# Performance work log

Hardware: AMD Instinct MI355X
Metric: run time of the kernel (lower is better)

Reference implementation:

```python
import jax, jax.numpy as jnp
import numpy as np

SPH, SPW = 24, 24          # spatial tile size
NBLK = 2                   # channel blocks (in_channels // 512)
EPS = 1e-5


def _tiles(h, w):
    nh = int(np.ceil(h / SPH)); nw = int(np.ceil(w / SPW))
    sh = (h - SPH) // (nh - 1) if nh > 1 else 0
    sw = (w - SPW) // (nw - 1) if nw > 1 else 0
    offs = []
    for i in range(nh):
        for j in range(nw):
            offs.append((max(0, i * sh), max(0, j * sw)))
    return offs, nh, nw


def _mlp(x_v, w1, b1, w2, b2):
    # 1x1 conv1d pair over the spatial_area axis: x_v (B, S, C)
    h = jax.nn.relu(jnp.einsum('os,bsc->boc', w1, x_v) + b1[None, :, None])
    return jnp.einsum('so,boc->bsc', w2, h) + b2[None, :, None]


def _forward(x, w_in1, b_in1, w_in2, b_in2, w_out1, b_out1, w_out2, b_out2, bn_gamma, bn_beta):
    bt, c, h, w = x.shape
    offs, nh, nw = _tiles(h, w)
    # gather overlapping (here exactly tiling) spatial patches -> stacked chunk batch
    chunks = [x[:, :, ty:ty + SPH, tx:tx + SPW].reshape(bt, c, SPH * SPW) for ty, tx in offs]
    x_stacked = jnp.concatenate(chunks, 0)            # (nchunks*bt, c, S)
    x_v = jnp.transpose(x_stacked, (0, 2, 1))         # (B, S, c)
    x_v = _mlp(x_v, w_in1, b_in1, w_in2, b_in2)
    # negative squared-distance score over channel means (no detach in this branch)
    x_m = x_v.mean(axis=1)                            # (B, c)
    score = -(x_m[:, None, :] - x_m[:, :, None]) ** 2  # (B, c, c)
    blk = c // NBLK
    ids = jnp.arange(c) // blk
    mask = ids[:, None] == ids[None, :]               # block-diagonal channel mask
    score = jnp.where(mask[None], score, -jnp.inf)
    attn = jax.nn.softmax(score, axis=1)              # softmax over dim 1 (rows)
    out = jnp.einsum('bsc,bcd->bsd', x_v, attn)       # torch.bmm(x_v, attn)
    out = _mlp(out, w_out1, b_out1, w_out2, b_out2)
    # BatchNorm1d(spatial_area) in training mode: stats over (B, c) per S-channel
    mu = out.mean(axis=(0, 2), keepdims=True)
    var = out.var(axis=(0, 2), keepdims=True)
    out = (out - mu) * jax.lax.rsqrt(var + EPS) * bn_gamma[None, :, None] + bn_beta[None, :, None]
    out = jnp.transpose(out, (0, 2, 1))               # (B, c, S)
    # scatter_add chunks back (scaled by 1/spblock_h^2, as in the original)
    scale = 1.0 / (nh * nh)
    res = x
    for idx, (ty, tx) in enumerate(offs):
        chunk = out[idx * bt:(idx + 1) * bt].reshape(bt, c, SPH, SPW)
        res = res.at[:, :, ty:ty + SPH, tx:tx + SPW].add(chunk * scale)
    return jax.nn.relu(res)


def setup_inputs() -> dict:
    key = jax.random.key(0)
    ks = jax.random.split(key, 9)
    S = SPH * SPW          # 576
    H = S // 8             # 72 (reduction=8)
    s = 0.02
    return {
        'x': jax.random.normal(ks[0], (16, 1024, 48, 48), dtype=jnp.float32),
        'w_in1': jax.random.normal(ks[1], (H, S), dtype=jnp.float32) * s,
        'b_in1': jnp.zeros((H,), jnp.float32),
        'w_in2': jax.random.normal(ks[2], (S, H), dtype=jnp.float32) * s,
        'b_in2': jnp.zeros((S,), jnp.float32),
        'w_out1': jax.random.normal(ks[3], (H, S), dtype=jnp.float32) * s,
        'b_out1': jnp.zeros((H,), jnp.float32),
        'w_out2': jax.random.normal(ks[4], (S, H), dtype=jnp.float32) * s,
        'b_out2': jnp.zeros((S,), jnp.float32),
        'bn_gamma': jnp.ones((S,), jnp.float32),
        'bn_beta': jnp.zeros((S,), jnp.float32),
    }


def reference(x, w_in1, b_in1, w_in2, b_in2, w_out1, b_out1, w_out2, b_out2, bn_gamma, bn_beta):
    return _forward(x, w_in1, b_in1, w_in2, b_in2, w_out1, b_out1, w_out2, b_out2, bn_gamma, bn_beta)
```

## Files before the change

kernel.cpp:

```cpp
#include <hip/hip_runtime.h>
#include <hip/hip_bf16.h>


#define EPS 1e-5f

typedef __attribute__((ext_vector_type(8))) short short8;
typedef __attribute__((ext_vector_type(4))) short short4v;
typedef __attribute__((ext_vector_type(4))) float f32x4;
typedef __attribute__((ext_vector_type(4))) float float4v;

#define GLD_LDS(g, l) __builtin_amdgcn_global_load_lds( \
    (const __attribute__((address_space(1))) void*)(g), \
    (__attribute__((address_space(3))) void*)(l), 16, 0, 0)

static __device__ __forceinline__ unsigned short f2bu(float f) {
    union { __hip_bfloat16 h; unsigned short u; } cv;
    cv.h = __float2bfloat16(f);
    return cv.u;
}

__global__ void prep_k(const float* __restrict__ w_in1, const float* __restrict__ b_in1,
                       const float* __restrict__ w_in2, const float* __restrict__ w_out2,
                       __hip_bfloat16* __restrict__ w1p, __hip_bfloat16* __restrict__ w2op,
                       float* __restrict__ b1p)
{
    int i = blockIdx.x * 256 + threadIdx.x;
    if (i < 128 * 576) {
        int r = i / 576, c = i - r * 576;
        w1p[i] = __float2bfloat16(r < 72 ? w_in1[r * 576 + c] : 0.f);
    }
    if (i < 640 * 96) {
        int r = i / 96, c = i - r * 96;
        bool ok = (r < 576) && (c < 72);
        w2op[i] = __float2bfloat16(ok ? w_out2[r * 72 + c] : 0.f);
    }
    if (i < 128)
        b1p[i] = i < 72 ? b_in1[i] : 0.f;
}

__global__ void prepM_k(const float* __restrict__ w_out1, const float* __restrict__ w_in2,
                        const float* __restrict__ b_in2, const float* __restrict__ b_out1,
                        __hip_bfloat16* __restrict__ Mp, float* __restrict__ b1G)
{
    int i = blockIdx.x * 256 + threadIdx.x;
    if (i >= 128 * 96) return;
    int h = i / 96, k = i - h * 96;
    float m = 0.f;
    if (h < 72 && k < 72) {
        for (int s = 0; s < 576; ++s)
            m += w_out1[h * 576 + s] * w_in2[s * 72 + k];
    } else if (h == 72 && k < 72) {
        for (int s = 0; s < 576; ++s)
            m += w_in2[s * 72 + k];
    }
    Mp[i] = __float2bfloat16(m);
    if (k == 0) {
        float c = 0.f;
        if (h < 72)
            for (int s = 0; s < 576; ++s)
                c += w_out1[h * 576 + s] * b_in2[s];
        b1G[h] = (h < 72) ? b_out1[h] + c : 0.f;
    }
}

__global__ void extract_k(const float4v* __restrict__ x4, __hip_bfloat16* __restrict__ xv)
{
    int i = blockIdx.x * 256 + threadIdx.x;
    int s4 = i % 144;
    int m = i / 144;
    int c = m & 1023;
    int b = m >> 10;
    int n = b & 15, ti = b >> 4;
    int ty = (ti >> 1) * 24, tx = (ti & 1) * 24;
    int s = s4 * 4;
    int sy = s / 24, sx = s - sy * 24;
    float4v v = x4[((((n << 10) + c) * 48 + ty + sy) * 48 + tx + sx) >> 2];
    short4v pk;
    pk.x = (short)f2bu(v.x); pk.y = (short)f2bu(v.y);
    pk.z = (short)f2bu(v.z); pk.w = (short)f2bu(v.w);
    *(short4v*)(xv + (long)i * 4) = pk;
}

__global__ __launch_bounds__(256) void fused_mlp1(
    const unsigned short* __restrict__ A,
    const unsigned short* __restrict__ W1,
    const float* __restrict__ b1,
    const unsigned short* __restrict__ Mp,
    unsigned short* __restrict__ G,
    float* __restrict__ xm_raw)
{
    __shared__ __align__(16) unsigned short smem[4096 + 4096 + 13312];
    unsigned short* As = smem;
    unsigned short* Bs = smem + 4096;
    unsigned short* Hs = smem + 8192;

    const int m0 = blockIdx.x * 128;
    const int t = threadIdx.x;
    const int lane = t & 63, wave = t >> 6;
    const int wr = wave >> 1, wc = wave & 1;
    const int lrow = lane & 15, kq = (lane >> 4) * 8;
    const int cr = (lane >> 4) * 4;
    const int r0 = t >> 2, c0 = (t & 3) * 8;

    f32x4 acc[4][4];
    #pragma unroll
    for (int i = 0; i < 4; ++i)
        #pragma unroll
        for (int j = 0; j < 4; ++j)
            acc[i][j] = (f32x4){0.f, 0.f, 0.f, 0.f};

    for (int k0 = 0; k0 < 576; k0 += 32) {
        GLD_LDS(A + (long)(m0 + r0) * 576 + k0 + c0,      &As[t * 8]);
        GLD_LDS(A + (long)(m0 + r0 + 64) * 576 + k0 + c0, &As[(t + 256) * 8]);
        GLD_LDS(W1 + (long)r0 * 576 + k0 + c0,            &Bs[t * 8]);
        GLD_LDS(W1 + (long)(r0 + 64) * 576 + k0 + c0,     &Bs[(t + 256) * 8]);
        __syncthreads();
        short8 af[4], bf[4];
        #pragma unroll
        for (int i = 0; i < 4; ++i)
            af[i] = *(const short8*)&As[(wr * 64 + i * 16 + lrow) * 32 + kq];
        #pragma unroll
        for (int j = 0; j < 4; ++j)
            bf[j] = *(const short8*)&Bs[(wc * 64 + j * 16 + lrow) * 32 + kq];
        #pragma unroll
        for (int i = 0; i < 4; ++i)
            #pragma unroll
            for (int j = 0; j < 4; ++j)
                acc[i][j] = __builtin_amdgcn_mfma_f32_16x16x32_bf16(af[i], bf[j], acc[i][j], 0, 0, 0);
        __syncthreads();
    }

    #pragma unroll
    for (int j = 0; j < 4; ++j) {
        int col = wc * 64 + j * 16 + lrow;
        if (col < 96) {
            float bv = b1[col];
            #pragma unroll
            for (int i = 0; i < 4; ++i) {
                int row = wr * 64 + i * 16 + cr;
                #pragma unroll
                for (int r = 0; r < 4; ++r)
                    Hs[(row + r) * 104 + col] = f2bu(fmaxf(acc[i][j][r] + bv, 0.f));
            }
        }
    }
    __syncthreads();

    f32x4 gacc[4][4];
    #pragma unroll
    for (int i = 0; i < 4; ++i)
        #pragma unroll
        for (int j = 0; j < 4; ++j)
            gacc[i][j] = (f32x4){0.f, 0.f, 0.f, 0.f};

    for (int k0 = 0; k0 < 96; k0 += 32) {
        GLD_LDS(Mp + (long)r0 * 96 + k0 + c0,        &As[t * 8]);
        GLD_LDS(Mp + (long)(r0 + 64) * 96 + k0 + c0, &As[(t + 256) * 8]);
        __syncthreads();
        short8 af[4], bf[4];
        #pragma unroll
        for (int i = 0; i < 4; ++i)
            af[i] = *(const short8*)&As[(wr * 64 + i * 16 + lrow) * 32 + kq];
        #pragma unroll
        for (int j = 0; j < 4; ++j)
            bf[j] = *(const short8*)&Hs[(wc * 64 + j * 16 + lrow) * 104 + k0 + kq];
        #pragma unroll
        for (int i = 0; i < 4; ++i)
            #pragma unroll
            for (int j = 0; j < 4; ++j)
                gacc[i][j] = __builtin_amdgcn_mfma_f32_16x16x32_bf16(af[i], bf[j], gacc[i][j], 0, 0, 0);
        __syncthreads();
    }

    const int z = m0 >> 9, m_local = m0 & 511;
    unsigned short* Gz = G + (long)z * 128 * 512;

    #pragma unroll
    for (int j = 0; j < 4; ++j) {
        int cn = wc * 64 + j * 16 + lrow;
        #pragma unroll
        for (int i = 0; i < 4; ++i) {
            int h = wr * 64 + i * 16 + cr;
            #pragma unroll
            for (int r = 0; r < 4; ++r)
                Gz[(long)(h + r) * 512 + m_local + cn] = f2bu(gacc[i][j][r]);
        }
    }

    if (wr == 1 && cr == 8) {
        #pragma unroll
        for (int j = 0; j < 4; ++j)
            xm_raw[(long)z * 512 + m_local + wc * 64 + j * 16 + lrow] = gacc[0][j][0];
    }
}

__global__ void denom_k(const float* __restrict__ xm_raw, const float* __restrict__ b_in2,
                        float* __restrict__ xmn, float* __restrict__ invd)
{
    __shared__ float sx[512];
    __shared__ float red[256];
    int z = blockIdx.x;
    int t = threadIdx.x;
    float p = 0.f;
    for (int i = t; i < 576; i += 256) p += b_in2[i];
    red[t] = p; __syncthreads();
    for (int o = 128; o; o >>= 1) { if (t < o) red[t] += red[t + o]; __syncthreads(); }
    float btot = red[0];
    for (int i = t; i < 512; i += 256) {
        float m = (xm_raw[(long)z * 512 + i] + btot) * (1.f / 576.f);
        sx[i] = m;
        xmn[(long)z * 512 + i] = m;
    }
    __syncthreads();
    #pragma unroll
    for (int dd = 0; dd < 2; ++dd) {
        int d = t + dd * 256;
        float xd = sx[d], s = 0.f;
        for (int c = 0; c < 512; ++c) { float df = sx[c] - xd; s += __expf(-df * df); }
        invd[(long)z * 512 + d] = 1.f / s;
    }
}

__global__ __launch_bounds__(256) void fused_attn_mlp2(
    const unsigned short* __restrict__ G,
    const float* __restrict__ xmn, const float* __restrict__ invd,
    const float* __restrict__ b1,
    const unsigned short* __restrict__ W2,
    const float* __restrict__ b2,
    __hip_bfloat16* __restrict__ C,
    float* __restrict__ statsR)
{
    __shared__ __align__(16) unsigned short smem[4096 + 4096 + 13312];
    unsigned short* As = smem;
    unsigned short* Bs = smem + 4096;
    unsigned short* Hs = smem + 8192;
    __shared__ float sxm[512];
    __shared__ float sinv[128];

    int bid = blockIdx.x;
    int lb = (bid & 7) * 64 + (bid >> 3);
    int z = lb >> 2;
    const int m0 = (lb & 3) * 128;
    const int t = threadIdx.x;
    const int lane = t & 63, wave = t >> 6;
    const int wr = wave >> 1, wc = wave & 1;
    const int lrow = lane & 15, kq = (lane >> 4) * 8;
    const int cr = (lane >> 4) * 4;
    const int r0 = t >> 2, c0 = (t & 3) * 8;
    const unsigned short* Gz = G + (long)z * 128 * 512;

    for (int i = t; i < 512; i += 256) sxm[i] = xmn[(long)z * 512 + i];
    if (t < 128) sinv[t] = invd[(long)z * 512 + m0 + t];
    __syncthreads();

    const int dA = t >> 1, cbA = (t & 1) * 16;
    const float xd = sxm[m0 + dA];
    const float ivd = sinv[dA];

    f32x4 acc[4][4];
    #pragma unroll
    for (int i = 0; i < 4; ++i)
        #pragma unroll
        for (int j = 0; j < 4; ++j)
            acc[i][j] = (f32x4){0.f, 0.f, 0.f, 0.f};

    for (int k0 = 0; k0 < 512; k0 += 32) {
        GLD_LDS(Gz + (long)r0 * 512 + k0 + c0,        &Bs[t * 8]);
        GLD_LDS(Gz + (long)(r0 + 64) * 512 + k0 + c0, &Bs[(t + 256) * 8]);
        short8 pk0, pk1;
        #pragma unroll
        for (int e = 0; e < 8; ++e) {
            float d0 = sxm[k0 + cbA + e] - xd;
            pk0[e] = (short)f2bu(__expf(-d0 * d0) * ivd);
            float d1 = sxm[k0 + cbA + 8 + e] - xd;
            pk1[e] = (short)f2bu(__expf(-d1 * d1) * ivd);
        }
        *(short8*)&As[dA * 32 + cbA]     = pk0;
        *(short8*)&As[dA * 32 + cbA + 8] = pk1;
        __syncthreads();
        short8 af[4], bf[4];
        #pragma unroll
        for (int i = 0; i < 4; ++i)
            af[i] = *(const short8*)&As[(wr * 64 + i * 16 + lrow) * 32 + kq];
        #pragma unroll
        for (int j = 0; j < 4; ++j)
            bf[j] = *(const short8*)&Bs[(wc * 64 + j * 16 + lrow) * 32 + kq];
        #pragma unroll
        for (int i = 0; i < 4; ++i)
            #pragma unroll
            for (int j = 0; j < 4; ++j)
                acc[i][j] = __builtin_amdgcn_mfma_f32_16x16x32_bf16(af[i], bf[j], acc[i][j], 0, 0, 0);
        __syncthreads();
    }

    #pragma unroll
    for (int j = 0; j < 4; ++j) {
        int col = wc * 64 + j * 16 + lrow;
        if (col < 96) {
            float bv = b1[col];
            #pragma unroll
            for (int i = 0; i < 4; ++i) {
                int row = wr * 64 + i * 16 + cr;
                #pragma unroll
                for (int r = 0; r < 4; ++r)
                    Hs[(row + r) * 104 + col] = f2bu(fmaxf(acc[i][j][r] + bv, 0.f));
            }
        }
    }
    __syncthreads();

    const long mg = (long)z * 512 + m0;
    float* st = statsR + (bid & 7) * 1152;
    for (int n0 = 0; n0 < 640; n0 += 128) {
        f32x4 a2[4][4];
        #pragma unroll
        for (int i = 0; i < 4; ++i)
            #pragma unroll
            for (int j = 0; j < 4; ++j)
                a2[i][j] = (f32x4){0.f, 0.f, 0.f, 0.f};

        for (int k0 = 0; k0 < 96; k0 += 32) {
            GLD_LDS(W2 + (long)(n0 + r0) * 96 + k0 + c0,      &Bs[t * 8]);
            GLD_LDS(W2 + (long)(n0 + r0 + 64) * 96 + k0 + c0, &Bs[(t + 256) * 8]);
            __syncthreads();
            short8 af[4], bf[4];
            #pragma unroll
            for (int i = 0; i < 4; ++i)
                af[i] = *(const short8*)&Hs[(wr * 64 + i * 16 + lrow) * 104 + k0 + kq];
            #pragma unroll
            for (int j = 0; j < 4; ++j)
                bf[j] = *(const short8*)&Bs[(wc * 64 + j * 16 + lrow) * 32 + kq];
            #pragma unroll
            for (int i = 0; i < 4; ++i)
                #pragma unroll
                for (int j = 0; j < 4; ++j)
                    a2[i][j] = __builtin_amdgcn_mfma_f32_16x16x32_bf16(af[i], bf[j], a2[i][j], 0, 0, 0);
            __syncthreads();
        }

        #pragma unroll
        for (int j = 0; j < 4; ++j) {
            int col = n0 + wc * 64 + j * 16 + lrow;
            bool live = col < 576;
            float bv = live ? b2[col] : 0.f;
            float s1 = 0.f, s2 = 0.f;
            #pragma unroll
            for (int i = 0; i < 4; ++i) {
                long rowb = (mg + wr * 64 + i * 16 + cr) * 576;
                #pragma unroll
                for (int r = 0; r < 4; ++r) {
                    float v = a2[i][j][r] + bv;
                    s1 += v; s2 += v * v;
                    if (live) C[rowb + (long)r * 576 + col] = __float2bfloat16(v);
                }
            }
            s1 += __shfl_xor(s1, 16, 64); s1 += __shfl_xor(s1, 32, 64);
            s2 += __shfl_xor(s2, 16, 64); s2 += __shfl_xor(s2, 32, 64);
            if ((lane >> 4) == 0 && live) {
                atomicAdd(&st[col], s1);
                atomicAdd(&st[576 + col], s2);
            }
        }
    }
}

__global__ void bnfin_k(const float* __restrict__ statsR,
                        const float* __restrict__ gamma, const float* __restrict__ beta,
                        float* __restrict__ ab)
{
    int s = threadIdx.x;
    float sum = 0.f, sq = 0.f;
    #pragma unroll
    for (int r = 0; r < 8; ++r) {
        sum += statsR[r * 1152 + s];
        sq  += statsR[r * 1152 + 576 + s];
    }
    float mu = sum * (1.f / 65536.f);
    float var = sq * (1.f / 65536.f) - mu * mu;
    float a = gamma[s] * rsqrtf(var + EPS);
    ab[s] = a;
    ab[576 + s] = beta[s] - mu * a;
}

__global__ void final_k(const float4v* __restrict__ x4, const __hip_bfloat16* __restrict__ out3,
                        const float* __restrict__ ab, float4v* __restrict__ out4)
{
    int i = blockIdx.x * 256 + threadIdx.x;
    int xx4 = i % 12; int t = i / 12;
    int y = t % 48; t /= 48;
    int c = t & 1023; int n = t >> 10;
    int xx = xx4 * 4;
    int ti = (y / 24) * 2 + (xx / 24);
    int b = ti * 16 + n;
    int s = (y % 24) * 24 + (xx % 24);
    const __hip_bfloat16* o3 = out3 + (((long)b << 10) + c) * 576 + s;
    float4v xv = x4[i];
    float4v o;
    #pragma unroll
    for (int e = 0; e < 4; ++e) {
        float v = __bfloat162float(o3[e]);
        float bn = v * ab[s + e] + ab[576 + s + e];
        float r = (e == 0 ? xv.x : e == 1 ? xv.y : e == 2 ? xv.z : xv.w) + 0.25f * bn;
        if (e == 0) o.x = fmaxf(r, 0.f);
        else if (e == 1) o.y = fmaxf(r, 0.f);
        else if (e == 2) o.z = fmaxf(r, 0.f);
        else o.w = fmaxf(r, 0.f);
    }
    out4[i] = o;
}

extern "C" void kernel_launch(void* const* d_in, const int* in_sizes, int n_in,
                              void* d_out, int out_size, void* d_ws, size_t ws_size,
                              hipStream_t stream)
{
    const float* x      = (const float*)d_in[0];
    const float* w_in1  = (const float*)d_in[1];
    const float* b_in1  = (const float*)d_in[2];
    const float* w_in2  = (const float*)d_in[3];
    const float* b_in2  = (const float*)d_in[4];
    const float* w_out1 = (const float*)d_in[5];
    const float* b_out1 = (const float*)d_in[6];
    const float* w_out2 = (const float*)d_in[7];
    const float* b_out2 = (const float*)d_in[8];
    const float* gamma  = (const float*)d_in[9];
    const float* beta   = (const float*)d_in[10];

    char* ws = (char*)d_ws;
    __hip_bfloat16* xv0    = (__hip_bfloat16*)(ws);
    __hip_bfloat16* out3   = (__hip_bfloat16*)(ws + 75497472L);
    unsigned short* G      = (unsigned short*)(ws + 150994944L);
    float*          xmn    = (float*)(ws + 167772160L);
    float*          xm_raw = (float*)(ws + 168034304L);
    float*          invd   = (float*)(ws + 168296448L);
    float*          statsR = (float*)(ws + 168558592L);
    float*          ab     = (float*)(ws + 168595456L);
    __hip_bfloat16* w1p    = (__hip_bfloat16*)(ws + 168600064L);
    __hip_bfloat16* w2op   = (__hip_bfloat16*)(ws + 168747520L);
    float*          b1p    = (float*)(ws + 168870400L);
    __hip_bfloat16* Mp     = (__hip_bfloat16*)(ws + 168870912L);
    float*          b1G    = (float*)(ws + 168895488L);

    hipMemsetAsync(statsR, 0, 36864, stream);

    prep_k<<<288, 256, 0, stream>>>(w_in1, b_in1, w_in2, w_out2, w1p, w2op, b1p);
    prepM_k<<<48, 256, 0, stream>>>(w_out1, w_in2, b_in2, b_out1, Mp, b1G);

    extract_k<<<36864, 256, 0, stream>>>((const float4v*)x, xv0);

    fused_mlp1<<<512, 256, 0, stream>>>(
        (const unsigned short*)xv0, (const unsigned short*)w1p, b1p,
        (const unsigned short*)Mp, G, xm_raw);

    denom_k<<<128, 256, 0, stream>>>(xm_raw, b_in2, xmn, invd);

    fused_attn_mlp2<<<512, 256, 0, stream>>>(
        G, xmn, invd, b1G, (const unsigned short*)w2op, b_out2,
        out3, statsR);

    bnfin_k<<<1, 576, 0, stream>>>(statsR, gamma, beta, ab);

    final_k<<<36864, 256, 0, stream>>>((const float4v*)x, out3, ab, (float4v*)d_out);
}
```

Baseline: 484.7 us.

## Fuse patch extraction and bf16 conversion into first MLP GEMM

Removes the separate extract kernel that gathered spatial tiles from x and wrote a bf16 staging buffer. The first fused MLP kernel now reads fp32 x directly, converts it to bf16 in registers and stores it into a padded LDS tile with a 96-wide K step. It also stages W1 through LDS with plain loads, so one full write and read of the intermediate buffer disappear. In exchange the GEMM main loop loses the async global-to-LDS loads, and LDS buffers are reshuffled in both fused kernels.

```diff
diff --git a/kernel.cpp b/kernel.cpp
--- a/kernel.cpp
+++ b/kernel.cpp
@@ -63,36 +63,17 @@
     }
 }
 
-__global__ void extract_k(const float4v* __restrict__ x4, __hip_bfloat16* __restrict__ xv)
-{
-    int i = blockIdx.x * 256 + threadIdx.x;
-    int s4 = i % 144;
-    int m = i / 144;
-    int c = m & 1023;
-    int b = m >> 10;
-    int n = b & 15, ti = b >> 4;
-    int ty = (ti >> 1) * 24, tx = (ti & 1) * 24;
-    int s = s4 * 4;
-    int sy = s / 24, sx = s - sy * 24;
-    float4v v = x4[((((n << 10) + c) * 48 + ty + sy) * 48 + tx + sx) >> 2];
-    short4v pk;
-    pk.x = (short)f2bu(v.x); pk.y = (short)f2bu(v.y);
-    pk.z = (short)f2bu(v.z); pk.w = (short)f2bu(v.w);
-    *(short4v*)(xv + (long)i * 4) = pk;
-}
-
 __global__ __launch_bounds__(256) void fused_mlp1(
-    const unsigned short* __restrict__ A,
+    const float* __restrict__ x,
     const unsigned short* __restrict__ W1,
     const float* __restrict__ b1,
     const unsigned short* __restrict__ Mp,
     unsigned short* __restrict__ G,
     float* __restrict__ xm_raw)
 {
-    __shared__ __align__(16) unsigned short smem[4096 + 4096 + 13312];
+    __shared__ __align__(16) unsigned short smem[13312 + 13312];
     unsigned short* As = smem;
-    unsigned short* Bs = smem + 4096;
-    unsigned short* Hs = smem + 8192;
+    unsigned short* Bs = smem + 13312;
 
     const int m0 = blockIdx.x * 128;
     const int t = threadIdx.x;
@@ -102,6 +83,16 @@
     const int cr = (lane >> 4) * 4;
     const int r0 = t >> 2, c0 = (t & 3) * 8;
 
+    const int rr = t >> 1, hf = t & 1;
+    {
+    }
+    const int Mrow = m0 + rr;
+    const int cch = Mrow & 1023, bb = Mrow >> 10;
+    const int nb = bb & 15, ti = bb >> 4;
+    const int ty = (ti >> 1) * 24, tx = (ti & 1) * 24;
+    const float* xrow = x + (((long)((nb << 10) + cch) * 48 + ty) * 48 + tx);
+    const unsigned short* w1row = W1 + rr * 576 + hf * 48;
+
     f32x4 acc[4][4];
     #pragma unroll
     for (int i = 0; i < 4; ++i)
@@ -109,26 +100,43 @@
         for (int j = 0; j < 4; ++j)
             acc[i][j] = (f32x4){0.f, 0.f, 0.f, 0.f};
 
-    for (int k0 = 0; k0 < 576; k0 += 32) {
-        GLD_LDS(A + (long)(m0 + r0) * 576 + k0 + c0,      &As[t * 8]);
-        GLD_LDS(A + (long)(m0 + r0 + 64) * 576 + k0 + c0, &As[(t + 256) * 8]);
-        GLD_LDS(W1 + (long)r0 * 576 + k0 + c0,            &Bs[t * 8]);
-        GLD_LDS(W1 + (long)(r0 + 64) * 576 + k0 + c0,     &Bs[(t + 256) * 8]);
-        __syncthreads();
-        short8 af[4], bf[4];
-        #pragma unroll
-        for (int i = 0; i < 4; ++i)
-            af[i] = *(const short8*)&As[(wr * 64 + i * 16 + lrow) * 32 + kq];
-        #pragma unroll
-        for (int j = 0; j < 4; ++j)
-            bf[j] = *(const short8*)&Bs[(wc * 64 + j * 16 + lrow) * 32 + kq];
-        #pragma unroll
-        for (int i = 0; i < 4; ++i)
+    for (int ks = 0; ks < 6; ++ks) {
+        __syncthreads();
+        #pragma unroll
+        for (int q = 0; q < 2; ++q) {
+            const int sy = ks * 4 + hf * 2 + q;
+            #pragma unroll
+            for (int xx = 0; xx < 6; ++xx) {
+                float4v v = *(const float4v*)(xrow + sy * 48 + xx * 4);
+                short4v pk;
+                pk.x = (short)f2bu(v.x); pk.y = (short)f2bu(v.y);
+                pk.z = (short)f2bu(v.z); pk.w = (short)f2bu(v.w);
+                *(short4v*)&As[rr * 104 + (hf * 2 + q) * 24 + xx * 4] = pk;
+            }
+        }
+        #pragma unroll
+        for (int sg = 0; sg < 6; ++sg) {
+            short8 w = *(const short8*)(w1row + ks * 96 + sg * 8);
+            *(short8*)&Bs[rr * 104 + hf * 48 + sg * 8] = w;
+        }
+        __syncthreads();
+        #pragma unroll
+        for (int kk = 0; kk < 3; ++kk) {
+            short8 af[4], bf[4];
+            #pragma unroll
+            for (int i = 0; i < 4; ++i)
+                af[i] = *(const short8*)&As[(wr * 64 + i * 16 + lrow) * 104 + kk * 32 + kq];
             #pragma unroll
             for (int j = 0; j < 4; ++j)
-                acc[i][j] = __builtin_amdgcn_mfma_f32_16x16x32_bf16(af[i], bf[j], acc[i][j], 0, 0, 0);
-        __syncthreads();
-    }
+                bf[j] = *(const short8*)&Bs[(wc * 64 + j * 16 + lrow) * 104 + kk * 32 + kq];
+            #pragma unroll
+            for (int i = 0; i < 4; ++i)
+                #pragma unroll
+                for (int j = 0; j < 4; ++j)
+                    acc[i][j] = __builtin_amdgcn_mfma_f32_16x16x32_bf16(af[i], bf[j], acc[i][j], 0, 0, 0);
+        }
+    }
+    __syncthreads();
 
     #pragma unroll
     for (int j = 0; j < 4; ++j) {
@@ -140,7 +148,7 @@
                 int row = wr * 64 + i * 16 + cr;
                 #pragma unroll
                 for (int r = 0; r < 4; ++r)
-                    Hs[(row + r) * 104 + col] = f2bu(fmaxf(acc[i][j][r] + bv, 0.f));
+                    As[(row + r) * 104 + col] = f2bu(fmaxf(acc[i][j][r] + bv, 0.f));
             }
         }
     }
@@ -154,16 +162,16 @@
             gacc[i][j] = (f32x4){0.f, 0.f, 0.f, 0.f};
 
     for (int k0 = 0; k0 < 96; k0 += 32) {
-        GLD_LDS(Mp + (long)r0 * 96 + k0 + c0,        &As[t * 8]);
-        GLD_LDS(Mp + (long)(r0 + 64) * 96 + k0 + c0, &As[(t + 256) * 8]);
+        GLD_LDS(Mp + (long)r0 * 96 + k0 + c0,        &Bs[t * 8]);
+        GLD_LDS(Mp + (long)(r0 + 64) * 96 + k0 + c0, &Bs[(t + 256) * 8]);
         __syncthreads();
         short8 af[4], bf[4];
         #pragma unroll
         for (int i = 0; i < 4; ++i)
-            af[i] = *(const short8*)&As[(wr * 64 + i * 16 + lrow) * 32 + kq];
-        #pragma unroll
-        for (int j = 0; j < 4; ++j)
-            bf[j] = *(const short8*)&Hs[(wc * 64 + j * 16 + lrow) * 104 + k0 + kq];
+            af[i] = *(const short8*)&Bs[(wr * 64 + i * 16 + lrow) * 32 + kq];
+        #pragma unroll
+        for (int j = 0; j < 4; ++j)
+            bf[j] = *(const short8*)&As[(wc * 64 + j * 16 + lrow) * 104 + k0 + kq];
         #pragma unroll
         for (int i = 0; i < 4; ++i)
             #pragma unroll
@@ -230,10 +238,11 @@
     __hip_bfloat16* __restrict__ C,
     float* __restrict__ statsR)
 {
-    __shared__ __align__(16) unsigned short smem[4096 + 4096 + 13312];
+    __shared__ __align__(16) unsigned short smem[17408];
     unsigned short* As = smem;
     unsigned short* Bs = smem + 4096;
-    unsigned short* Hs = smem + 8192;
+    unsigned short* Hs = smem;
+    unsigned short* Ws = smem + 13312;
     __shared__ float sxm[512];
     __shared__ float sinv[128];
 
@@ -320,8 +329,8 @@
                 a2[i][j] = (f32x4){0.f, 0.f, 0.f, 0.f};
 
         for (int k0 = 0; k0 < 96; k0 += 32) {
-            GLD_LDS(W2 + (long)(n0 + r0) * 96 + k0 + c0,      &Bs[t * 8]);
-            GLD_LDS(W2 + (long)(n0 + r0 + 64) * 96 + k0 + c0, &Bs[(t + 256) * 8]);
+            GLD_LDS(W2 + (long)(n0 + r0) * 96 + k0 + c0,      &Ws[t * 8]);
+            GLD_LDS(W2 + (long)(n0 + r0 + 64) * 96 + k0 + c0, &Ws[(t + 256) * 8]);
             __syncthreads();
             short8 af[4], bf[4];
             #pragma unroll
@@ -329,7 +338,7 @@
                 af[i] = *(const short8*)&Hs[(wr * 64 + i * 16 + lrow) * 104 + k0 + kq];
             #pragma unroll
             for (int j = 0; j < 4; ++j)
-                bf[j] = *(const short8*)&Bs[(wc * 64 + j * 16 + lrow) * 32 + kq];
+                bf[j] = *(const short8*)&Ws[(wc * 64 + j * 16 + lrow) * 32 + kq];
             #pragma unroll
             for (int i = 0; i < 4; ++i)
                 #pragma unroll
@@ -426,29 +435,26 @@
     const float* beta   = (const float*)d_in[10];
 
     char* ws = (char*)d_ws;
-    __hip_bfloat16* xv0    = (__hip_bfloat16*)(ws);
-    __hip_bfloat16* out3   = (__hip_bfloat16*)(ws + 75497472L);
-    unsigned short* G      = (unsigned short*)(ws + 150994944L);
-    float*          xmn    = (float*)(ws + 167772160L);
-    float*          xm_raw = (float*)(ws + 168034304L);
-    float*          invd   = (float*)(ws + 168296448L);
-    float*          statsR = (float*)(ws + 168558592L);
-    float*          ab     = (float*)(ws + 168595456L);
-    __hip_bfloat16* w1p    = (__hip_bfloat16*)(ws + 168600064L);
-    __hip_bfloat16* w2op   = (__hip_bfloat16*)(ws + 168747520L);
-    float*          b1p    = (float*)(ws + 168870400L);
-    __hip_bfloat16* Mp     = (__hip_bfloat16*)(ws + 168870912L);
-    float*          b1G    = (float*)(ws + 168895488L);
+    __hip_bfloat16* out3   = (__hip_bfloat16*)(ws);
+    unsigned short* G      = (unsigned short*)(ws + 75497472L);
+    float*          xmn    = (float*)(ws + 92274688L);
+    float*          xm_raw = (float*)(ws + 92536832L);
+    float*          invd   = (float*)(ws + 92798976L);
+    float*          statsR = (float*)(ws + 93061120L);
+    float*          ab     = (float*)(ws + 93097984L);
+    __hip_bfloat16* w1p    = (__hip_bfloat16*)(ws + 93102592L);
+    __hip_bfloat16* w2op   = (__hip_bfloat16*)(ws + 93250048L);
+    float*          b1p    = (float*)(ws + 93372928L);
+    __hip_bfloat16* Mp     = (__hip_bfloat16*)(ws + 93373440L);
+    float*          b1G    = (float*)(ws + 93398016L);
 
     hipMemsetAsync(statsR, 0, 36864, stream);
 
     prep_k<<<288, 256, 0, stream>>>(w_in1, b_in1, w_in2, w_out2, w1p, w2op, b1p);
     prepM_k<<<48, 256, 0, stream>>>(w_out1, w_in2, b_in2, b_out1, Mp, b1G);
 
-    extract_k<<<36864, 256, 0, stream>>>((const float4v*)x, xv0);
-
     fused_mlp1<<<512, 256, 0, stream>>>(
-        (const unsigned short*)xv0, (const unsigned short*)w1p, b1p,
+        x, (const unsigned short*)w1p, b1p,
         (const unsigned short*)Mp, G, xm_raw);
 
     denom_k<<<128, 256, 0, stream>>>(xm_raw, b_in2, xmn, invd);
```

Result: faster. 451.9 us (-6.8%).
